# Kernel tuning notes

Hardware: AMD Instinct MI355X
Metric: run time of the kernel (lower is better)

## Reference

```python
import jax, jax.numpy as jnp
import numpy as np

N_NODES = 100000


def gcn_conv(x, W, b, src, dst, num_nodes):
    """PyG GCNConv: out = D^{-1/2} (A + I) D^{-1/2} (x W) + b, messages src->dst."""
    h = x @ W  # [N, out]
    # degree with self-loops (edge weight 1)
    deg = jax.ops.segment_sum(jnp.ones(src.shape[0], dtype=x.dtype), dst,
                              num_segments=num_nodes) + 1.0
    dinv = jax.lax.rsqrt(deg)  # [N]
    norm = dinv[src] * dinv[dst]  # [E]
    msg = h[src] * norm[:, None]  # gather + scale, [E, out]
    agg = jax.ops.segment_sum(msg, dst, num_segments=num_nodes)
    # self-loop term: norm_ii = dinv[i]^2
    agg = agg + h * (dinv * dinv)[:, None]
    return agg + b


def setup_inputs() -> dict:
    key = jax.random.key(0)
    ks = jax.random.split(key, 9)
    N, F_in, H1, H2, C = N_NODES, 128, 64, 32, 10
    E = 3200000
    feature = jax.random.normal(ks[0], (N, F_in), dtype=jnp.float32)
    edge_index = jax.random.randint(ks[1], (2, E), 0, N, dtype=jnp.int64)
    def glorot(k, shape):
        lim = np.sqrt(6.0 / (shape[0] + shape[1]))
        return jax.random.uniform(k, shape, jnp.float32, -lim, lim)
    return {
        "feature": feature,
        "edge_index": edge_index,
        "W1": glorot(ks[2], (F_in, H1)),
        "b1": jnp.zeros((H1,), jnp.float32),
        "W2": glorot(ks[3], (H1, H2)),
        "b2": jnp.zeros((H2,), jnp.float32),
        "Wc": glorot(ks[4], (H2, C)),
        "bc": jnp.zeros((C,), jnp.float32),
    }


def reference(feature, edge_index, W1, b1, W2, b2, Wc, bc):
    src, dst = edge_index[0], edge_index[1]
    x = gcn_conv(feature, W1, b1, src, dst, N_NODES)
    x = jax.nn.relu(x)
    # dropout is identity in eval mode
    x = gcn_conv(x, W2, b2, src, dst, N_NODES)
    x = jax.nn.relu(x)
    logits = x @ Wc + bc
    return jax.nn.log_softmax(logits, axis=1)
```

## Files before the change

### kernel.cpp

```cpp
#include <hip/hip_runtime.h>

#define N_NODES 100000
#define F_IN 128
#define H1 64
#define H2 32
#define NCLS 10

#define BS_N 256
#define NBUCK ((N_NODES + BS_N - 1) / BS_N)
#define LCAP 32
#define MCAP 12288
#define OVCAP 2048
#define STCAP 12288
#define BIN_WG 256
#define SENT 0xFFFFFFFFu

__device__ __forceinline__ unsigned short f2bf(float f) {
    unsigned int u = __float_as_uint(f);
    return (unsigned short)((u + 0x7fffu + ((u >> 16) & 1u)) >> 16);
}
__device__ __forceinline__ void accp(float* a, unsigned int u) {
    a[0] += __uint_as_float(u << 16);
    a[1] += __uint_as_float(u & 0xffff0000u);
}
__device__ __forceinline__ void accp4(float* a, uint4 v) {
    accp(a + 0, v.x); accp(a + 2, v.y); accp(a + 4, v.z); accp(a + 6, v.w);
}

__global__ __launch_bounds__(512) void bin_kernel(const int* __restrict__ src,
                                                  const int* __restrict__ dst, int E,
                                                  unsigned int* __restrict__ gcur,
                                                  unsigned int* __restrict__ mainr,
                                                  unsigned int* __restrict__ ovcnt,
                                                  unsigned int* __restrict__ ovbuf) {
    __shared__ unsigned int buf[NBUCK][LCAP];
    __shared__ int cnt[NBUCK];
    int tid = threadIdx.x;
    for (int b = tid; b < NBUCK; b += 512) cnt[b] = 0;

    int chunk = (E + gridDim.x - 1) / gridDim.x;
    int e_lo = blockIdx.x * chunk;
    int e_hi = min(e_lo + chunk, E);

    int d0 = 0, s0 = 0, d1 = 0, s1 = 0;
    {
        int ea = e_lo + tid, eb = e_lo + 512 + tid;
        if (ea < e_hi) { d0 = dst[ea]; s0 = src[ea]; }
        if (eb < e_hi) { d1 = dst[eb]; s1 = src[eb]; }
    }
    __syncthreads();

    for (int base = e_lo; base < e_hi; base += 1024) {
        if (base + tid < e_hi) {
            int b = d0 >> 8;
            unsigned int en = ((unsigned int)s0 << 8) | (unsigned int)(d0 & 255);
            int p = atomicAdd(&cnt[b], 1);
            if (p < LCAP) buf[b][p] = en;
            else {
                unsigned int op = atomicAdd(&ovcnt[b * 16], 1u);
                if (op < OVCAP) ovbuf[(size_t)b * OVCAP + op] = en;
            }
        }
        if (base + 512 + tid < e_hi) {
            int b = d1 >> 8;
            unsigned int en = ((unsigned int)s1 << 8) | (unsigned int)(d1 & 255);
            int p = atomicAdd(&cnt[b], 1);
            if (p < LCAP) buf[b][p] = en;
            else {
                unsigned int op = atomicAdd(&ovcnt[b * 16], 1u);
                if (op < OVCAP) ovbuf[(size_t)b * OVCAP + op] = en;
            }
        }
        __syncthreads();
        {
            int nb = base + 1024;
            int ea = nb + tid, eb = nb + 512 + tid;
            if (ea < e_hi) { d0 = dst[ea]; s0 = src[ea]; }
            if (eb < e_hi) { d1 = dst[eb]; s1 = src[eb]; }
        }
        for (int b = tid; b < NBUCK; b += 512) {
            int c = cnt[b]; if (c > LCAP) c = LCAP;
            int nf = c & ~15;
            if (nf) {
                unsigned int gb = atomicAdd(&gcur[b * 16], (unsigned int)nf);
                if (gb + (unsigned)nf <= MCAP) {
                    for (int k = 0; k < nf; k += 4) {
                        uint4 v = make_uint4(buf[b][k], buf[b][k + 1],
                                             buf[b][k + 2], buf[b][k + 3]);
                        *(uint4*)&mainr[(size_t)b * MCAP + gb + k] = v;
                    }
                } else {
                    unsigned int op = atomicAdd(&ovcnt[b * 16], (unsigned int)nf);
                    for (int k = 0; k < nf; ++k)
                        if (op + k < OVCAP) ovbuf[(size_t)b * OVCAP + op + k] = buf[b][k];
                }
                int rem = c - nf;
                for (int k = 0; k < rem; ++k) buf[b][k] = buf[b][nf + k];
                cnt[b] = rem;
            } else {
                cnt[b] = c;
            }
        }
        __syncthreads();
    }
    for (int b = tid; b < NBUCK; b += 512) {
        int c = cnt[b]; if (c > LCAP) c = LCAP;
        if (c) {
            int cp = (c + 15) & ~15;
            for (int k = c; k < cp; ++k) buf[b][k] = SENT;
            unsigned int gb = atomicAdd(&gcur[b * 16], (unsigned int)cp);
            if (gb + (unsigned)cp <= MCAP) {
                for (int k = 0; k < cp; k += 4) {
                    uint4 v = make_uint4(buf[b][k], buf[b][k + 1],
                                         buf[b][k + 2], buf[b][k + 3]);
                    *(uint4*)&mainr[(size_t)b * MCAP + gb + k] = v;
                }
            } else {
                unsigned int op = atomicAdd(&ovcnt[b * 16], (unsigned int)c);
                for (int k = 0; k < c; ++k)
                    if (op + k < OVCAP) ovbuf[(size_t)b * OVCAP + op + k] = buf[b][k];
            }
        }
    }
}

__global__ __launch_bounds__(256) void build_kernel(const unsigned int* __restrict__ gcur,
                                                    unsigned int* __restrict__ mainr,
                                                    const unsigned int* __restrict__ ovcnt,
                                                    const unsigned int* __restrict__ ovbuf,
                                                    float* __restrict__ dinv,
                                                    int* __restrict__ row_start,
                                                    int* __restrict__ row_end) {
    __shared__ unsigned int stage[STCAP];
    __shared__ int degl[BS_N];
    __shared__ int rs_l[BS_N];
    __shared__ int curl[BS_N];
    __shared__ int wtot[4];
    int b = blockIdx.x;
    int tid = threadIdx.x;

    int cm = (int)gcur[b * 16]; if (cm > MCAP) cm = MCAP;
    for (int i = tid; i < cm; i += 256) stage[i] = mainr[(size_t)b * MCAP + i];
    int co = (int)ovcnt[b * 16]; if (co > OVCAP) co = OVCAP;
    for (int i = tid; i < co; i += 256) {
        int p = cm + i;
        if (p < STCAP) stage[p] = ovbuf[(size_t)b * OVCAP + i];
    }
    int c = cm + co; if (c > STCAP) c = STCAP;
    degl[tid] = 0;
    __syncthreads();

    for (int i = tid; i < c; i += 256) {
        unsigned int en = stage[i];
        if (en != SENT) atomicAdd(&degl[en & 255], 1);
    }
    __syncthreads();

    int lane = tid & 63, w = tid >> 6;
    int d = degl[tid];
    int x = d;
    #pragma unroll
    for (int off = 1; off < 64; off <<= 1) {
        int y = __shfl_up(x, off);
        if (lane >= off) x += y;
    }
    if (lane == 63) wtot[w] = x;
    __syncthreads();
    int pbase = 0;
    #pragma unroll
    for (int k = 0; k < 4; ++k) if (k < w) pbase += wtot[k];
    rs_l[tid] = pbase + x - d;
    curl[tid] = 0;
    __syncthreads();

    size_t gbase = (size_t)b * MCAP;
    for (int i = tid; i < c; i += 256) {
        unsigned int en = stage[i];
        if (en != SENT) {
            int dl = en & 255;
            int p = atomicAdd(&curl[dl], 1);
            mainr[gbase + rs_l[dl] + p] = en >> 8;
        }
    }
    int node = b * BS_N + tid;
    if (node < N_NODES) {
        int deg = degl[tid];
        dinv[node] = rsqrtf((float)deg + 1.0f);
        row_start[node] = (int)gbase + rs_l[tid];
        row_end[node] = (int)gbase + rs_l[tid] + deg;
    }
}

__global__ __launch_bounds__(256) void gemm1_kernel(const float* __restrict__ X,
                                                    const float* __restrict__ W,
                                                    const float* __restrict__ dinv,
                                                    unsigned short* __restrict__ H) {
    __shared__ float Xs[64][68];
    __shared__ float Ws[F_IN * H1];
    int r0 = blockIdx.x * 64;
    const float4* W4 = (const float4*)W;
    float4* Ws4 = (float4*)Ws;
    for (int i = threadIdx.x; i < F_IN * H1 / 4; i += 256) Ws4[i] = W4[i];

    int tx = threadIdx.x & 15;
    int ty = threadIdx.x >> 4;
    float acc[4][4] = {};

    for (int kh = 0; kh < 2; ++kh) {
        __syncthreads();
        for (int it = 0; it < 4; ++it) {
            int idx = threadIdx.x + it * 256;
            int r = idx >> 4, k4 = idx & 15;
            int row = r0 + r;
            float4 v = (row < N_NODES)
                ? ((const float4*)X)[(size_t)row * 32 + kh * 16 + k4]
                : make_float4(0.f, 0.f, 0.f, 0.f);
            *(float4*)&Xs[r][k4 * 4] = v;
        }
        __syncthreads();
        #pragma unroll 8
        for (int k = 0; k < 64; ++k) {
            float4 wb = *(const float4*)&Ws[(kh * 64 + k) * H1 + tx * 4];
            float xa0 = Xs[ty * 4 + 0][k];
            float xa1 = Xs[ty * 4 + 1][k];
            float xa2 = Xs[ty * 4 + 2][k];
            float xa3 = Xs[ty * 4 + 3][k];
            acc[0][0] += xa0 * wb.x; acc[0][1] += xa0 * wb.y; acc[0][2] += xa0 * wb.z; acc[0][3] += xa0 * wb.w;
            acc[1][0] += xa1 * wb.x; acc[1][1] += xa1 * wb.y; acc[1][2] += xa1 * wb.z; acc[1][3] += xa1 * wb.w;
            acc[2][0] += xa2 * wb.x; acc[2][1] += xa2 * wb.y; acc[2][2] += xa2 * wb.z; acc[2][3] += xa2 * wb.w;
            acc[3][0] += xa3 * wb.x; acc[3][1] += xa3 * wb.y; acc[3][2] += xa3 * wb.z; acc[3][3] += xa3 * wb.w;
        }
    }
    #pragma unroll
    for (int i = 0; i < 4; ++i) {
        int row = r0 + ty * 4 + i;
        if (row < N_NODES) {
            float dv = dinv[row];
            unsigned int lo = (unsigned int)f2bf(acc[i][0] * dv) |
                              ((unsigned int)f2bf(acc[i][1] * dv) << 16);
            unsigned int hi = (unsigned int)f2bf(acc[i][2] * dv) |
                              ((unsigned int)f2bf(acc[i][3] * dv) << 16);
            *(uint2*)&H[(size_t)row * H1 + tx * 4] = make_uint2(lo, hi);
        }
    }
}

__global__ __launch_bounds__(256) void gemm2_kernel(const float* __restrict__ X,
                                                    const float* __restrict__ W,
                                                    const float* __restrict__ dinv,
                                                    unsigned short* __restrict__ H) {
    __shared__ float Xs[64][68];
    __shared__ float Ws[H1 * H2];
    int r0 = blockIdx.x * 64;
    const float4* W4 = (const float4*)W;
    float4* Ws4 = (float4*)Ws;
    for (int i = threadIdx.x; i < H1 * H2 / 4; i += 256) Ws4[i] = W4[i];
    for (int it = 0; it < 4; ++it) {
        int idx = threadIdx.x + it * 256;
        int r = idx >> 4, k4 = idx & 15;
        int row = r0 + r;
        float4 v = (row < N_NODES)
            ? ((const float4*)X)[(size_t)row * 16 + k4]
            : make_float4(0.f, 0.f, 0.f, 0.f);
        *(float4*)&Xs[r][k4 * 4] = v;
    }
    __syncthreads();
    int tx = threadIdx.x & 15;
    int ty = threadIdx.x >> 4;
    float acc[4][2] = {};
    #pragma unroll 8
    for (int k = 0; k < 64; ++k) {
        float2 wb = *(const float2*)&Ws[k * H2 + tx * 2];
        float xa0 = Xs[ty * 4 + 0][k];
        float xa1 = Xs[ty * 4 + 1][k];
        float xa2 = Xs[ty * 4 + 2][k];
        float xa3 = Xs[ty * 4 + 3][k];
        acc[0][0] += xa0 * wb.x; acc[0][1] += xa0 * wb.y;
        acc[1][0] += xa1 * wb.x; acc[1][1] += xa1 * wb.y;
        acc[2][0] += xa2 * wb.x; acc[2][1] += xa2 * wb.y;
        acc[3][0] += xa3 * wb.x; acc[3][1] += xa3 * wb.y;
    }
    #pragma unroll
    for (int i = 0; i < 4; ++i) {
        int row = r0 + ty * 4 + i;
        if (row < N_NODES) {
            float dv = dinv[row];
            unsigned int v = (unsigned int)f2bf(acc[i][0] * dv) |
                             ((unsigned int)f2bf(acc[i][1] * dv) << 16);
            *(unsigned int*)&H[(size_t)row * H2 + tx * 2] = v;
        }
    }
}

__global__ __launch_bounds__(256) void pull1_kernel(const unsigned short* __restrict__ h,
                                                    const unsigned int* __restrict__ csr,
                                                    const int* __restrict__ row_start,
                                                    const int* __restrict__ row_end,
                                                    const float* __restrict__ dinv,
                                                    const float* __restrict__ b,
                                                    float* __restrict__ xout) {
    int wave = (blockIdx.x * 256 + threadIdx.x) >> 6;
    int lane = threadIdx.x & 63;
    int g = lane >> 3;
    int sub = lane & 7;
    int i = wave;
    int e0 = row_start[i], e1 = row_end[i];
    float acc[8] = {};
    int e = e0;
    for (; e + 16 <= e1; e += 16) {
        int s0 = csr[e + g];
        int s1 = csr[e + 8 + g];
        uint4 v0 = *(const uint4*)&h[(size_t)s0 * H1 + sub * 8];
        uint4 v1 = *(const uint4*)&h[(size_t)s1 * H1 + sub * 8];
        accp4(acc, v0);
        accp4(acc, v1);
    }
    if (e + 8 <= e1) {
        int s = csr[e + g];
        uint4 v = *(const uint4*)&h[(size_t)s * H1 + sub * 8];
        accp4(acc, v);
        e += 8;
    }
    if (e < e1) {
        int idx = e + g;
        if (idx < e1) {
            int s = csr[idx];
            uint4 v = *(const uint4*)&h[(size_t)s * H1 + sub * 8];
            accp4(acc, v);
        }
    }
    #pragma unroll
    for (int m = 8; m < 64; m <<= 1) {
        #pragma unroll
        for (int j = 0; j < 8; ++j) acc[j] += __shfl_xor(acc[j], m);
    }
    if (g == 0) {
        float di = dinv[i];
        uint4 sv = *(const uint4*)&h[(size_t)i * H1 + sub * 8];
        accp4(acc, sv);
        float4 o0, o1;
        o0.x = fmaxf(di * acc[0] + b[sub * 8 + 0], 0.0f);
        o0.y = fmaxf(di * acc[1] + b[sub * 8 + 1], 0.0f);
        o0.z = fmaxf(di * acc[2] + b[sub * 8 + 2], 0.0f);
        o0.w = fmaxf(di * acc[3] + b[sub * 8 + 3], 0.0f);
        o1.x = fmaxf(di * acc[4] + b[sub * 8 + 4], 0.0f);
        o1.y = fmaxf(di * acc[5] + b[sub * 8 + 5], 0.0f);
        o1.z = fmaxf(di * acc[6] + b[sub * 8 + 6], 0.0f);
        o1.w = fmaxf(di * acc[7] + b[sub * 8 + 7], 0.0f);
        *(float4*)&xout[(size_t)i * H1 + sub * 8] = o0;
        *(float4*)&xout[(size_t)i * H1 + sub * 8 + 4] = o1;
    }
}

__global__ __launch_bounds__(256) void pull2_kernel(const unsigned short* __restrict__ h,
                                                    const unsigned int* __restrict__ csr,
                                                    const int* __restrict__ row_start,
                                                    const int* __restrict__ row_end,
                                                    const float* __restrict__ dinv,
                                                    const float* __restrict__ b,
                                                    float* __restrict__ xout) {
    int wave = (blockIdx.x * 256 + threadIdx.x) >> 6;
    int lane = threadIdx.x & 63;
    int g = lane >> 2;
    int sub = lane & 3;
    int i = wave;
    int e0 = row_start[i], e1 = row_end[i];
    float acc[8] = {};
    int e = e0;
    for (; e + 32 <= e1; e += 32) {
        int s0 = csr[e + g];
        int s1 = csr[e + 16 + g];
        uint4 v0 = *(const uint4*)&h[(size_t)s0 * H2 + sub * 8];
        uint4 v1 = *(const uint4*)&h[(size_t)s1 * H2 + sub * 8];
        accp4(acc, v0);
        accp4(acc, v1);
    }
    if (e + 16 <= e1) {
        int s = csr[e + g];
        uint4 v = *(const uint4*)&h[(size_t)s * H2 + sub * 8];
        accp4(acc, v);
        e += 16;
    }
    if (e < e1) {
        int idx = e + g;
        if (idx < e1) {
            int s = csr[idx];
            uint4 v = *(const uint4*)&h[(size_t)s * H2 + sub * 8];
            accp4(acc, v);
        }
    }
    #pragma unroll
    for (int m = 4; m < 64; m <<= 1) {
        #pragma unroll
        for (int j = 0; j < 8; ++j) acc[j] += __shfl_xor(acc[j], m);
    }
    if (g == 0) {
        float di = dinv[i];
        uint4 sv = *(const uint4*)&h[(size_t)i * H2 + sub * 8];
        accp4(acc, sv);
        float4 o0, o1;
        o0.x = fmaxf(di * acc[0] + b[sub * 8 + 0], 0.0f);
        o0.y = fmaxf(di * acc[1] + b[sub * 8 + 1], 0.0f);
        o0.z = fmaxf(di * acc[2] + b[sub * 8 + 2], 0.0f);
        o0.w = fmaxf(di * acc[3] + b[sub * 8 + 3], 0.0f);
        o1.x = fmaxf(di * acc[4] + b[sub * 8 + 4], 0.0f);
        o1.y = fmaxf(di * acc[5] + b[sub * 8 + 5], 0.0f);
        o1.z = fmaxf(di * acc[6] + b[sub * 8 + 6], 0.0f);
        o1.w = fmaxf(di * acc[7] + b[sub * 8 + 7], 0.0f);
        *(float4*)&xout[(size_t)i * H2 + sub * 8] = o0;
        *(float4*)&xout[(size_t)i * H2 + sub * 8 + 4] = o1;
    }
}

__global__ __launch_bounds__(256) void final_kernel(const float* __restrict__ X2,
                                                    const float* __restrict__ Wc,
                                                    const float* __restrict__ bc,
                                                    float* __restrict__ out) {
    __shared__ float Ws[H2 * NCLS];
    __shared__ float bs[NCLS];
    for (int idx = threadIdx.x; idx < H2 * NCLS; idx += 256) Ws[idx] = Wc[idx];
    if (threadIdx.x < NCLS) bs[threadIdx.x] = bc[threadIdx.x];
    __syncthreads();
    int i = blockIdx.x * blockDim.x + threadIdx.x;
    if (i >= N_NODES) return;
    float x[H2];
    #pragma unroll
    for (int k = 0; k < H2; ++k) x[k] = X2[(size_t)i * H2 + k];
    float lg[NCLS];
    #pragma unroll
    for (int c = 0; c < NCLS; ++c) {
        float acc = bs[c];
        #pragma unroll
        for (int k = 0; k < H2; ++k) acc += x[k] * Ws[k * NCLS + c];
        lg[c] = acc;
    }
    float m = lg[0];
    #pragma unroll
    for (int c = 1; c < NCLS; ++c) m = fmaxf(m, lg[c]);
    float s = 0.0f;
    #pragma unroll
    for (int c = 0; c < NCLS; ++c) s += expf(lg[c] - m);
    float lse = m + logf(s);
    #pragma unroll
    for (int c = 0; c < NCLS; ++c) out[(size_t)i * NCLS + c] = lg[c] - lse;
}

extern "C" void kernel_launch(void* const* d_in, const int* in_sizes, int n_in,
                              void* d_out, int out_size, void* d_ws, size_t ws_size,
                              hipStream_t stream) {
    const float* feature = (const float*)d_in[0];
    const int*   eidx    = (const int*)d_in[1];
    const float* W1      = (const float*)d_in[2];
    const float* b1      = (const float*)d_in[3];
    const float* W2      = (const float*)d_in[4];
    const float* b2      = (const float*)d_in[5];
    const float* Wc      = (const float*)d_in[6];
    const float* bc      = (const float*)d_in[7];
    float* out = (float*)d_out;

    const int E = in_sizes[1] / 2;
    const int* src = eidx;
    const int* dst = eidx + E;

    float*          ws        = (float*)d_ws;
    float*          dinv      = ws;
    int*            row_start = (int*)(dinv + N_NODES);
    int*            row_end   = row_start + N_NODES;
    unsigned int*   gcur      = (unsigned int*)(row_end + N_NODES);
    unsigned int*   ovcnt     = gcur + (size_t)NBUCK * 16;
    unsigned int*   ovbuf     = ovcnt + (size_t)NBUCK * 16;
    unsigned int*   mainr     = ovbuf + (size_t)NBUCK * OVCAP;
    unsigned short* h1b       = (unsigned short*)(mainr + (size_t)NBUCK * MCAP);
    float*          x1        = (float*)(h1b + (size_t)N_NODES * H1);
    unsigned short* h2b       = h1b;
    float*          x2        = x1;

    hipMemsetAsync(gcur, 0, (size_t)NBUCK * 32 * sizeof(unsigned int), stream);
    bin_kernel<<<BIN_WG, 512, 0, stream>>>(src, dst, E, gcur, mainr, ovcnt, ovbuf);
    build_kernel<<<NBUCK, 256, 0, stream>>>(gcur, mainr, ovcnt, ovbuf,
                                            dinv, row_start, row_end);

    gemm1_kernel<<<(N_NODES + 63) / 64, 256, 0, stream>>>(feature, W1, dinv, h1b);
    {
        unsigned int grid = (unsigned int)(((size_t)N_NODES * 64 + 255) / 256);
        pull1_kernel<<<grid, 256, 0, stream>>>(h1b, mainr, row_start, row_end, dinv, b1, x1);
    }

    gemm2_kernel<<<(N_NODES + 63) / 64, 256, 0, stream>>>(x1, W2, dinv, h2b);
    {
        unsigned int grid = (unsigned int)(((size_t)N_NODES * 64 + 255) / 256);
        pull2_kernel<<<grid, 256, 0, stream>>>(h2b, mainr, row_start, row_end, dinv, b2, x2);
    }

    final_kernel<<<(N_NODES + 255) / 256, 256, 0, stream>>>(x2, Wc, bc, out);
}
```

Baseline: 316.1 us.

## Store layer-1 output in bf16, vectorize edge loads, widen build workgroups

```diff
diff --git a/kernel.cpp b/kernel.cpp
--- a/kernel.cpp
+++ b/kernel.cpp
@@ -18,6 +18,9 @@
 __device__ __forceinline__ unsigned short f2bf(float f) {
     unsigned int u = __float_as_uint(f);
     return (unsigned short)((u + 0x7fffu + ((u >> 16) & 1u)) >> 16);
+}
+__device__ __forceinline__ float bf2f(unsigned short u) {
+    return __uint_as_float((unsigned int)u << 16);
 }
 __device__ __forceinline__ void accp(float* a, unsigned int u) {
     a[0] += __uint_as_float(u << 16);
@@ -44,39 +47,47 @@
 
     int d0 = 0, s0 = 0, d1 = 0, s1 = 0;
     {
-        int ea = e_lo + tid, eb = e_lo + 512 + tid;
-        if (ea < e_hi) { d0 = dst[ea]; s0 = src[ea]; }
-        if (eb < e_hi) { d1 = dst[eb]; s1 = src[eb]; }
+        int ea = e_lo + 2 * tid;
+        if (ea < e_hi) {
+            int2 dd = *(const int2*)&dst[ea];
+            int2 ss = *(const int2*)&src[ea];
+            d0 = dd.x; s0 = ss.x; d1 = dd.y; s1 = ss.y;
+        }
     }
     __syncthreads();
 
     for (int base = e_lo; base < e_hi; base += 1024) {
-        if (base + tid < e_hi) {
-            int b = d0 >> 8;
-            unsigned int en = ((unsigned int)s0 << 8) | (unsigned int)(d0 & 255);
-            int p = atomicAdd(&cnt[b], 1);
-            if (p < LCAP) buf[b][p] = en;
-            else {
-                unsigned int op = atomicAdd(&ovcnt[b * 16], 1u);
-                if (op < OVCAP) ovbuf[(size_t)b * OVCAP + op] = en;
+        int ea = base + 2 * tid;
+        if (ea < e_hi) {
+            {
+                int b = d0 >> 8;
+                unsigned int en = ((unsigned int)s0 << 8) | (unsigned int)(d0 & 255);
+                int p = atomicAdd(&cnt[b], 1);
+                if (p < LCAP) buf[b][p] = en;
+                else {
+                    unsigned int op = atomicAdd(&ovcnt[b * 16], 1u);
+                    if (op < OVCAP) ovbuf[(size_t)b * OVCAP + op] = en;
+                }
             }
-        }
-        if (base + 512 + tid < e_hi) {
-            int b = d1 >> 8;
-            unsigned int en = ((unsigned int)s1 << 8) | (unsigned int)(d1 & 255);
-            int p = atomicAdd(&cnt[b], 1);
-            if (p < LCAP) buf[b][p] = en;
-            else {
-                unsigned int op = atomicAdd(&ovcnt[b * 16], 1u);
-                if (op < OVCAP) ovbuf[(size_t)b * OVCAP + op] = en;
+            if (ea + 1 < e_hi) {
+                int b = d1 >> 8;
+                unsigned int en = ((unsigned int)s1 << 8) | (unsigned int)(d1 & 255);
+                int p = atomicAdd(&cnt[b], 1);
+                if (p < LCAP) buf[b][p] = en;
+                else {
+                    unsigned int op = atomicAdd(&ovcnt[b * 16], 1u);
+                    if (op < OVCAP) ovbuf[(size_t)b * OVCAP + op] = en;
+                }
             }
         }
         __syncthreads();
         {
-            int nb = base + 1024;
-            int ea = nb + tid, eb = nb + 512 + tid;
-            if (ea < e_hi) { d0 = dst[ea]; s0 = src[ea]; }
-            if (eb < e_hi) { d1 = dst[eb]; s1 = src[eb]; }
+            int nb = base + 1024 + 2 * tid;
+            if (nb < e_hi) {
+                int2 dd = *(const int2*)&dst[nb];
+                int2 ss = *(const int2*)&src[nb];
+                d0 = dd.x; s0 = ss.x; d1 = dd.y; s1 = ss.y;
+            }
         }
         for (int b = tid; b < NBUCK; b += 512) {
             int c = cnt[b]; if (c > LCAP) c = LCAP;
@@ -124,7 +135,7 @@
     }
 }
 
-__global__ __launch_bounds__(256) void build_kernel(const unsigned int* __restrict__ gcur,
+__global__ __launch_bounds__(512) void build_kernel(const unsigned int* __restrict__ gcur,
                                                     unsigned int* __restrict__ mainr,
                                                     const unsigned int* __restrict__ ovcnt,
                                                     const unsigned int* __restrict__ ovbuf,
@@ -140,41 +151,45 @@
     int tid = threadIdx.x;
 
     int cm = (int)gcur[b * 16]; if (cm > MCAP) cm = MCAP;
-    for (int i = tid; i < cm; i += 256) stage[i] = mainr[(size_t)b * MCAP + i];
+    for (int i = tid; i < cm; i += 512) stage[i] = mainr[(size_t)b * MCAP + i];
     int co = (int)ovcnt[b * 16]; if (co > OVCAP) co = OVCAP;
-    for (int i = tid; i < co; i += 256) {
+    for (int i = tid; i < co; i += 512) {
         int p = cm + i;
         if (p < STCAP) stage[p] = ovbuf[(size_t)b * OVCAP + i];
     }
     int c = cm + co; if (c > STCAP) c = STCAP;
-    degl[tid] = 0;
+    if (tid < BS_N) degl[tid] = 0;
     __syncthreads();
 
-    for (int i = tid; i < c; i += 256) {
+    for (int i = tid; i < c; i += 512) {
         unsigned int en = stage[i];
         if (en != SENT) atomicAdd(&degl[en & 255], 1);
     }
     __syncthreads();
 
-    int lane = tid & 63, w = tid >> 6;
-    int d = degl[tid];
-    int x = d;
-    #pragma unroll
-    for (int off = 1; off < 64; off <<= 1) {
-        int y = __shfl_up(x, off);
-        if (lane >= off) x += y;
-    }
-    if (lane == 63) wtot[w] = x;
+    if (tid < 256) {
+        int lane = tid & 63, w = tid >> 6;
+        int d = degl[tid];
+        int x = d;
+        #pragma unroll
+        for (int off = 1; off < 64; off <<= 1) {
+            int y = __shfl_up(x, off);
+            if (lane >= off) x += y;
+        }
+        if (lane == 63) wtot[w] = x;
+        __syncthreads();
+        int pbase = 0;
+        #pragma unroll
+        for (int k = 0; k < 4; ++k) if (k < w) pbase += wtot[k];
+        rs_l[tid] = pbase + x - d;
+        curl[tid] = 0;
+    } else {
+        __syncthreads();
+    }
     __syncthreads();
-    int pbase = 0;
-    #pragma unroll
-    for (int k = 0; k < 4; ++k) if (k < w) pbase += wtot[k];
-    rs_l[tid] = pbase + x - d;
-    curl[tid] = 0;
-    __syncthreads();
 
     size_t gbase = (size_t)b * MCAP;
-    for (int i = tid; i < c; i += 256) {
+    for (int i = tid; i < c; i += 512) {
         unsigned int en = stage[i];
         if (en != SENT) {
             int dl = en & 255;
@@ -182,12 +197,14 @@
             mainr[gbase + rs_l[dl] + p] = en >> 8;
         }
     }
-    int node = b * BS_N + tid;
-    if (node < N_NODES) {
-        int deg = degl[tid];
-        dinv[node] = rsqrtf((float)deg + 1.0f);
-        row_start[node] = (int)gbase + rs_l[tid];
-        row_end[node] = (int)gbase + rs_l[tid] + deg;
+    if (tid < 256) {
+        int node = b * BS_N + tid;
+        if (node < N_NODES) {
+            int deg = degl[tid];
+            dinv[node] = rsqrtf((float)deg + 1.0f);
+            row_start[node] = (int)gbase + rs_l[tid];
+            row_end[node] = (int)gbase + rs_l[tid] + deg;
+        }
     }
 }
 
@@ -245,7 +262,7 @@
     }
 }
 
-__global__ __launch_bounds__(256) void gemm2_kernel(const float* __restrict__ X,
+__global__ __launch_bounds__(256) void gemm2_kernel(const unsigned short* __restrict__ X,
                                                     const float* __restrict__ W,
                                                     const float* __restrict__ dinv,
                                                     unsigned short* __restrict__ H) {
@@ -255,14 +272,20 @@
     const float4* W4 = (const float4*)W;
     float4* Ws4 = (float4*)Ws;
     for (int i = threadIdx.x; i < H1 * H2 / 4; i += 256) Ws4[i] = W4[i];
-    for (int it = 0; it < 4; ++it) {
+    for (int it = 0; it < 2; ++it) {
         int idx = threadIdx.x + it * 256;
-        int r = idx >> 4, k4 = idx & 15;
+        int r = idx >> 3, k8 = idx & 7;
         int row = r0 + r;
-        float4 v = (row < N_NODES)
-            ? ((const float4*)X)[(size_t)row * 16 + k4]
-            : make_float4(0.f, 0.f, 0.f, 0.f);
-        *(float4*)&Xs[r][k4 * 4] = v;
+        uint4 v = (row < N_NODES)
+            ? ((const uint4*)X)[(size_t)row * 8 + k8]
+            : make_uint4(0u, 0u, 0u, 0u);
+        float4 a, bb;
+        a.x = bf2f((unsigned short)(v.x & 0xffff)); a.y = bf2f((unsigned short)(v.x >> 16));
+        a.z = bf2f((unsigned short)(v.y & 0xffff)); a.w = bf2f((unsigned short)(v.y >> 16));
+        bb.x = bf2f((unsigned short)(v.z & 0xffff)); bb.y = bf2f((unsigned short)(v.z >> 16));
+        bb.z = bf2f((unsigned short)(v.w & 0xffff)); bb.w = bf2f((unsigned short)(v.w >> 16));
+        *(float4*)&Xs[r][k8 * 8] = a;
+        *(float4*)&Xs[r][k8 * 8 + 4] = bb;
     }
     __syncthreads();
     int tx = threadIdx.x & 15;
@@ -298,7 +321,7 @@
                                                     const int* __restrict__ row_end,
                                                     const float* __restrict__ dinv,
                                                     const float* __restrict__ b,
-                                                    float* __restrict__ xout) {
+                                                    unsigned short* __restrict__ xout) {
     int wave = (blockIdx.x * 256 + threadIdx.x) >> 6;
     int lane = threadIdx.x & 63;
     int g = lane >> 3;
@@ -338,17 +361,16 @@
         float di = dinv[i];
         uint4 sv = *(const uint4*)&h[(size_t)i * H1 + sub * 8];
         accp4(acc, sv);
-        float4 o0, o1;
-        o0.x = fmaxf(di * acc[0] + b[sub * 8 + 0], 0.0f);
-        o0.y = fmaxf(di * acc[1] + b[sub * 8 + 1], 0.0f);
-        o0.z = fmaxf(di * acc[2] + b[sub * 8 + 2], 0.0f);
-        o0.w = fmaxf(di * acc[3] + b[sub * 8 + 3], 0.0f);
-        o1.x = fmaxf(di * acc[4] + b[sub * 8 + 4], 0.0f);
-        o1.y = fmaxf(di * acc[5] + b[sub * 8 + 5], 0.0f);
-        o1.z = fmaxf(di * acc[6] + b[sub * 8 + 6], 0.0f);
-        o1.w = fmaxf(di * acc[7] + b[sub * 8 + 7], 0.0f);
-        *(float4*)&xout[(size_t)i * H1 + sub * 8] = o0;
-        *(float4*)&xout[(size_t)i * H1 + sub * 8 + 4] = o1;
+        float o[8];
+        #pragma unroll
+        for (int j = 0; j < 8; ++j)
+            o[j] = fmaxf(di * acc[j] + b[sub * 8 + j], 0.0f);
+        uint4 pk;
+        pk.x = (unsigned int)f2bf(o[0]) | ((unsigned int)f2bf(o[1]) << 16);
+        pk.y = (unsigned int)f2bf(o[2]) | ((unsigned int)f2bf(o[3]) << 16);
+        pk.z = (unsigned int)f2bf(o[4]) | ((unsigned int)f2bf(o[5]) << 16);
+        pk.w = (unsigned int)f2bf(o[6]) | ((unsigned int)f2bf(o[7]) << 16);
+        *(uint4*)&xout[(size_t)i * H1 + sub * 8] = pk;
     }
 }
 
@@ -471,22 +493,22 @@
     unsigned int*   ovbuf     = ovcnt + (size_t)NBUCK * 16;
     unsigned int*   mainr     = ovbuf + (size_t)NBUCK * OVCAP;
     unsigned short* h1b       = (unsigned short*)(mainr + (size_t)NBUCK * MCAP);
-    float*          x1        = (float*)(h1b + (size_t)N_NODES * H1);
+    unsigned short* x1b       = h1b + (size_t)N_NODES * H1;
     unsigned short* h2b       = h1b;
-    float*          x2        = x1;
+    float*          x2        = (float*)x1b;
 
     hipMemsetAsync(gcur, 0, (size_t)NBUCK * 32 * sizeof(unsigned int), stream);
     bin_kernel<<<BIN_WG, 512, 0, stream>>>(src, dst, E, gcur, mainr, ovcnt, ovbuf);
-    build_kernel<<<NBUCK, 256, 0, stream>>>(gcur, mainr, ovcnt, ovbuf,
+    build_kernel<<<NBUCK, 512, 0, stream>>>(gcur, mainr, ovcnt, ovbuf,
                                             dinv, row_start, row_end);
 
     gemm1_kernel<<<(N_NODES + 63) / 64, 256, 0, stream>>>(feature, W1, dinv, h1b);
     {
         unsigned int grid = (unsigned int)(((size_t)N_NODES * 64 + 255) / 256);
-        pull1_kernel<<<grid, 256, 0, stream>>>(h1b, mainr, row_start, row_end, dinv, b1, x1);
-    }
-
-    gemm2_kernel<<<(N_NODES + 63) / 64, 256, 0, stream>>>(x1, W2, dinv, h2b);
+        pull1_kernel<<<grid, 256, 0, stream>>>(h1b, mainr, row_start, row_end, dinv, b1, x1b);
+    }
+
+    gemm2_kernel<<<(N_NODES + 63) / 64, 256, 0, stream>>>(x1b, W2, dinv, h2b);
     {
         unsigned int grid = (unsigned int)(((size_t)N_NODES * 64 + 255) / 256);
         pull2_kernel<<<grid, 256, 0, stream>>>(h2b, mainr, row_start, row_end, dinv, b2, x2);
```

Measured after the change: 312.6 us. No clear change (-1.1%).
